# Kernel tuning notes

Hardware: AMD Instinct MI355X
Metric: run time of the kernel (lower is better)

Reference implementation:

```python
import jax, jax.numpy as jnp
import numpy as np

NUM_HEADS = 16
SOFTPLUS_EPS = 1e-4


def rotate_half(x):
    x1, x2 = jnp.split(x, 2, axis=-1)
    return jnp.concatenate((-x2, x1), axis=-1)


def setup_inputs() -> dict:
    key = jax.random.key(0)
    B, S, H = 1, 2048, 2048
    D = H // NUM_HEADS  # 128
    ks = jax.random.split(key, 5)
    hidden_states = jax.random.normal(ks[0], (B, S, H), dtype=jnp.float32)
    # standard RoPE tables: [S, D]
    inv_freq = 1.0 / (10000.0 ** (np.arange(0, D, 2, dtype=np.float32) / D))
    freqs = np.outer(np.arange(S, dtype=np.float32), inv_freq)  # [S, D/2]
    emb = np.concatenate([freqs, freqs], axis=-1)  # [S, D]
    cos = jnp.asarray(np.cos(emb), dtype=jnp.float32)
    sin = jnp.asarray(np.sin(emb), dtype=jnp.float32)
    std = 0.02
    w_q = jax.random.normal(ks[1], (2 * H, H), dtype=jnp.float32) * std
    w_k = jax.random.normal(ks[2], (2 * H, H), dtype=jnp.float32) * std
    w_v = jax.random.normal(ks[3], (H, H), dtype=jnp.float32) * std
    w_o = jax.random.normal(ks[4], (H, H), dtype=jnp.float32) * std
    return {"hidden_states": hidden_states, "cos": cos, "sin": sin,
            "w_q": w_q, "w_k": w_k, "w_v": w_v, "w_o": w_o}


def reference(hidden_states, cos, sin, w_q, w_k, w_v, w_o):
    B, S, H = hidden_states.shape
    NH = NUM_HEADS
    D = H // NH
    # projections (torch Linear: y = x @ W.T)
    q = (hidden_states @ w_q.T).reshape(B, S, NH, 2 * D).swapaxes(1, 2)  # [B,NH,S,2D]
    k = (hidden_states @ w_k.T).reshape(B, S, NH, 2 * D).swapaxes(1, 2)
    v = (hidden_states @ w_v.T).reshape(B, S, NH, D).swapaxes(1, 2)      # [B,NH,S,D]
    q_mu, q_sigma_raw = jnp.split(q, 2, axis=-1)
    k_mu, k_sigma_raw = jnp.split(k, 2, axis=-1)
    q_sigma = jax.nn.softplus(q_sigma_raw) + SOFTPLUS_EPS
    k_sigma = jax.nn.softplus(k_sigma_raw) + SOFTPLUS_EPS
    q_w = q_mu / jnp.sqrt(q_sigma)
    k_w = k_mu / jnp.sqrt(k_sigma)
    # RoPE on variance-weighted means; cos/sin [S,D] broadcast over [B,NH,S,D]
    q_w = q_w * cos + rotate_half(q_w) * sin
    k_w = k_w * cos + rotate_half(k_w) * sin
    q_sq = jnp.sum(q_w * q_w, axis=-1, keepdims=True)          # [B,NH,S,1]
    k_sq = jnp.sum(k_w * k_w, axis=-1, keepdims=True)          # [B,NH,S,1]
    dot = jnp.einsum('bhqd,bhkd->bhqk', q_w, k_w)              # [B,NH,S,S]
    weighted_dist = q_sq + jnp.swapaxes(k_sq, -2, -1) - 2.0 * dot
    log_det_q = jnp.sum(jnp.log(q_sigma), axis=-1, keepdims=True)
    log_det_k = jnp.sum(jnp.log(k_sigma), axis=-1, keepdims=True)
    log_det = log_det_q + jnp.swapaxes(log_det_k, -2, -1)
    attn_scores = -0.5 * (weighted_dist + log_det)
    attn_probs = jax.nn.softmax(attn_scores, axis=-1)
    attn_out = jnp.einsum('bhqk,bhkd->bhqd', attn_probs, v)    # [B,NH,S,D]
    attn_out = attn_out.swapaxes(1, 2).reshape(B, S, H)
    return attn_out @ w_o.T
```

## Files before the change

kernel.cpp:

```cpp
#include <hip/hip_runtime.h>
#include <stdint.h>

#define S_LEN 2048
#define HID   2048
#define NHEAD 16
#define HD    128
#define NQK   8192
#define K_HID 2048

typedef _Float16 f16x8 __attribute__((ext_vector_type(8)));
typedef float    f32x4 __attribute__((ext_vector_type(4)));

__device__ __forceinline__ unsigned short f2h(float f) {
    _Float16 h = (_Float16)f;
    union { _Float16 h; unsigned short u; } c; c.h = h;
    return c.u;
}
__device__ __forceinline__ float h2f(unsigned short b) {
    union { unsigned short u; _Float16 h; } c; c.u = b;
    return (float)c.h;
}
__device__ __forceinline__ float softplus_f(float x) {
    return (x > 20.f) ? x : log1pf(expf(x));
}
__device__ __forceinline__ void gload_lds16(const unsigned short* g, unsigned short* l) {
    __builtin_amdgcn_global_load_lds(
        (const __attribute__((address_space(1))) unsigned int*)g,
        (__attribute__((address_space(3))) unsigned int*)l, 16, 0, 0);
}

__global__ __launch_bounds__(256) void cast5(const float* __restrict__ hs,
                                             const float* __restrict__ wq,
                                             const float* __restrict__ wk,
                                             const float* __restrict__ wv,
                                             const float* __restrict__ wo,
                                             unsigned short* __restrict__ hs16,
                                             unsigned short* __restrict__ wqk16,
                                             unsigned short* __restrict__ wv16,
                                             unsigned short* __restrict__ wo16) {
    int b = blockIdx.x;
    const float* src;
    unsigned short* dst;
    int i;
    if (b < 4096)       { src = hs; dst = hs16;                          i = b; }
    else if (b < 12288) { src = wq; dst = wqk16;                         i = b - 4096; }
    else if (b < 20480) { src = wk; dst = wqk16 + (size_t)4096 * K_HID;  i = b - 12288; }
    else if (b < 24576) { src = wv; dst = wv16;                          i = b - 20480; }
    else                { src = wo; dst = wo16;                          i = b - 24576; }
    int idx = i * 256 + threadIdx.x;
    float4 v = ((const float4*)src)[idx];
    ushort4 o;
    o.x = f2h(v.x); o.y = f2h(v.y); o.z = f2h(v.z); o.w = f2h(v.w);
    ((ushort4*)dst)[idx] = o;
}

template <bool OUT_F16>
__device__ __forceinline__ void gemm_body(const unsigned short* __restrict__ A,
                                          const unsigned short* __restrict__ B,
                                          void* __restrict__ Cv,
                                          int m0, int n0, int N,
                                          unsigned short* As, unsigned short* Bs) {
    const int t    = threadIdx.x;
    const int wave = t >> 6;
    const int lane = t & 63;
    const int wm   = wave >> 1, wn = wave & 1;
    const int lrow = lane & 15, quad = lane >> 4;
    const int srow = lane >> 2;
    const int scol = (lane & 3) * 8;

    f32x4 acc[4][4];
    for (int i = 0; i < 4; ++i)
        for (int j = 0; j < 4; ++j)
            acc[i][j] = (f32x4){0.f, 0.f, 0.f, 0.f};

    for (int k0 = 0; k0 < K_HID; k0 += 32) {
        for (int c = 0; c < 2; ++c) {
            int ch = wave * 2 + c;
            int row = ch * 16 + srow;
            gload_lds16(A + (size_t)(m0 + row) * K_HID + k0 + scol, &As[ch * 512]);
            gload_lds16(B + (size_t)(n0 + row) * K_HID + k0 + scol, &Bs[ch * 512]);
        }
        __syncthreads();

        f16x8 af[4], bfr[4];
        for (int tm = 0; tm < 4; ++tm)
            af[tm]  = *(const f16x8*)(&As[(wm * 64 + tm * 16 + lrow) * 32 + quad * 8]);
        for (int tn = 0; tn < 4; ++tn)
            bfr[tn] = *(const f16x8*)(&Bs[(wn * 64 + tn * 16 + lrow) * 32 + quad * 8]);
        for (int tm = 0; tm < 4; ++tm)
            for (int tn = 0; tn < 4; ++tn)
                acc[tm][tn] = __builtin_amdgcn_mfma_f32_16x16x32_f16(af[tm], bfr[tn], acc[tm][tn], 0, 0, 0);
        __syncthreads();
    }

    for (int tm = 0; tm < 4; ++tm)
        for (int tn = 0; tn < 4; ++tn) {
            int col = n0 + wn * 64 + tn * 16 + lrow;
            for (int r = 0; r < 4; ++r) {
                int row = m0 + wm * 64 + tm * 16 + quad * 4 + r;
                if (OUT_F16)
                    ((unsigned short*)Cv)[(size_t)row * N + col] = f2h(acc[tm][tn][r]);
                else
                    ((float*)Cv)[(size_t)row * N + col] = acc[tm][tn][r];
            }
        }
}

__global__ __launch_bounds__(256) void gemm_qkv(const unsigned short* __restrict__ hs16,
                                                const unsigned short* __restrict__ wqk16,
                                                const unsigned short* __restrict__ wv16,
                                                unsigned short* __restrict__ qk16,
                                                unsigned short* __restrict__ Vt) {
    __shared__ __align__(16) unsigned short As[128 * 32];
    __shared__ __align__(16) unsigned short Bs[128 * 32];
    int b = blockIdx.x;
    if (b < 1024) {
        gemm_body<true>(hs16, wqk16, qk16, (b >> 6) * 128, (b & 63) * 128, NQK, As, Bs);
    } else {
        b -= 1024;
        gemm_body<true>(wv16, hs16, Vt, (b >> 4) * 128, (b & 15) * 128, S_LEN, As, Bs);
    }
}

template <bool OUT_F16>
__global__ __launch_bounds__(256) void gemm_nt_f16(const unsigned short* __restrict__ A,
                                                   const unsigned short* __restrict__ B,
                                                   void* __restrict__ Cv,
                                                   int M, int N, int Kd) {
    __shared__ __align__(16) unsigned short As[128 * 32];
    __shared__ __align__(16) unsigned short Bs[128 * 32];
    gemm_body<OUT_F16>(A, B, Cv, blockIdx.y * 128, blockIdx.x * 128, N, As, Bs);
}

__global__ __launch_bounds__(256) void prep_qk(const unsigned short* __restrict__ qk,
                                               const float* __restrict__ cosb,
                                               const float* __restrict__ sinb,
                                               unsigned short* __restrict__ Q16,
                                               unsigned short* __restrict__ K16,
                                               float* __restrict__ kbias) {
    int gid  = blockIdx.x * 4 + (threadIdx.x >> 6);
    int lane = threadIdx.x & 63;
    int h = gid >> 11;
    int s = gid & 2047;
    int d1 = lane, d2 = lane + 64;
    const unsigned short* row = qk + (size_t)s * NQK;
    float c1 = cosb[s * HD + d1], c2 = cosb[s * HD + d2];
    float s1 = sinb[s * HD + d1], s2 = sinb[s * HD + d2];
    size_t ob = ((size_t)h * S_LEN + s) * HD;

    {
        int base = h * 256;
        float mu1 = h2f(row[base + d1]),       mu2 = h2f(row[base + d2]);
        float sg1 = softplus_f(h2f(row[base + 128 + d1])) + 1e-4f;
        float sg2 = softplus_f(h2f(row[base + 128 + d2])) + 1e-4f;
        float w1 = mu1 * rsqrtf(sg1), w2 = mu2 * rsqrtf(sg2);
        float o1 = w1 * c1 - w2 * s1;
        float o2 = w2 * c2 + w1 * s2;
        Q16[ob + d1] = f2h(o1);
        Q16[ob + d2] = f2h(o2);
    }
    {
        int base = 4096 + h * 256;
        float mu1 = h2f(row[base + d1]),       mu2 = h2f(row[base + d2]);
        float sg1 = softplus_f(h2f(row[base + 128 + d1])) + 1e-4f;
        float sg2 = softplus_f(h2f(row[base + 128 + d2])) + 1e-4f;
        float w1 = mu1 * rsqrtf(sg1), w2 = mu2 * rsqrtf(sg2);
        float o1 = w1 * c1 - w2 * s1;
        float o2 = w2 * c2 + w1 * s2;
        unsigned short k1 = f2h(o1), k2 = f2h(o2);
        K16[ob + d1] = k1; K16[ob + d2] = k2;
        float r1 = h2f(k1), r2 = h2f(k2);
        float part = r1 * r1 + r2 * r2 + logf(sg1) + logf(sg2);
        for (int off = 32; off > 0; off >>= 1) part += __shfl_down(part, off);
        if (lane == 0) kbias[(size_t)h * S_LEN + s] = -0.5f * part;
    }
}

__global__ __launch_bounds__(256, 2) void flash_mfma(const unsigned short* __restrict__ Q16,
                                                     const unsigned short* __restrict__ K16,
                                                     const unsigned short* __restrict__ Vt,
                                                     const float* __restrict__ kbias,
                                                     unsigned short* __restrict__ OP,
                                                     float* __restrict__ ML) {
    constexpr int LV = 72;
    __shared__ __align__(16) unsigned short Khs[4 * 64 * 32];
    __shared__ __align__(16) unsigned short Vts[2 * 128 * 32];
    __shared__ __align__(16) unsigned short Ps[128 * LV];
    __shared__ float kb[64];

    const int t    = threadIdx.x;
    const int h    = blockIdx.y;
    const int q0   = blockIdx.x * 128;
    const int kz   = blockIdx.z;
    const int wave = t >> 6;
    const int lane = t & 63;
    const int lrow = lane & 15, quad = lane >> 4;
    const int srow = lane >> 2;
    const int scol = (lane & 3) * 8;

    f16x8 qf[2][4];
    for (int m = 0; m < 2; ++m) {
        size_t rb = ((size_t)h * S_LEN + q0 + wave * 32 + m * 16 + lrow) * HD;
        for (int kk = 0; kk < 4; ++kk)
            qf[m][kk] = *(const f16x8*)(Q16 + rb + kk * 32 + quad * 8);
    }

    float mrow[2][4], lsum[2][4];
    f32x4 Ofr[2][8];
    for (int m = 0; m < 2; ++m)
        for (int r = 0; r < 4; ++r) { mrow[m][r] = -INFINITY; lsum[m][r] = 0.f; }
    for (int m = 0; m < 2; ++m)
        for (int d = 0; d < 8; ++d) Ofr[m][d] = (f32x4){0.f, 0.f, 0.f, 0.f};

    const int kbeg = kz * 1024;
    for (int k0 = kbeg; k0 < kbeg + 1024; k0 += 64) {
        {
            const unsigned short* kgb = K16 + ((size_t)h * S_LEN + k0) * HD;
            const unsigned short* vgb = Vt + ((size_t)h * HD) * S_LEN + k0;
            for (int c = 0; c < 4; ++c) {
                int ch = wave * 4 + c;
                int kk = ch >> 2;
                int r  = (ch & 3) * 16 + srow;
                gload_lds16(kgb + (size_t)r * HD + kk * 32 + scol, &Khs[ch * 512]);
                int kc = ch >> 3;
                int r2 = (ch & 7) * 16 + srow;
                gload_lds16(vgb + (size_t)r2 * S_LEN + kc * 32 + scol, &Vts[ch * 512]);
            }
            if (t < 64) kb[t] = kbias[(size_t)h * S_LEN + k0 + t];
        }
        __syncthreads();

        f32x4 sc[2][4];
        for (int m = 0; m < 2; ++m)
            for (int nt = 0; nt < 4; ++nt) sc[m][nt] = (f32x4){0.f, 0.f, 0.f, 0.f};
        for (int kk = 0; kk < 4; ++kk)
            for (int nt = 0; nt < 4; ++nt) {
                f16x8 khf = *(const f16x8*)(&Khs[kk * 2048 + (nt * 16 + lrow) * 32 + quad * 8]);
                sc[0][nt] = __builtin_amdgcn_mfma_f32_16x16x32_f16(qf[0][kk], khf, sc[0][nt], 0, 0, 0);
                sc[1][nt] = __builtin_amdgcn_mfma_f32_16x16x32_f16(qf[1][kk], khf, sc[1][nt], 0, 0, 0);
            }
        float kbn[4] = {kb[lrow], kb[16 + lrow], kb[32 + lrow], kb[48 + lrow]};

        for (int m = 0; m < 2; ++m)
            for (int r = 0; r < 4; ++r) {
                float s0 = sc[m][0][r] + kbn[0];
                float s1 = sc[m][1][r] + kbn[1];
                float s2 = sc[m][2][r] + kbn[2];
                float s3 = sc[m][3][r] + kbn[3];
                float mx = fmaxf(fmaxf(s0, s1), fmaxf(s2, s3));
                mx = fmaxf(mx, __shfl_xor(mx, 1));
                mx = fmaxf(mx, __shfl_xor(mx, 2));
                mx = fmaxf(mx, __shfl_xor(mx, 4));
                mx = fmaxf(mx, __shfl_xor(mx, 8));
                float mnew  = fmaxf(mrow[m][r], mx);
                float alpha = __expf(mrow[m][r] - mnew);
                mrow[m][r] = mnew;
                float p0 = __expf(s0 - mnew);
                float p1 = __expf(s1 - mnew);
                float p2 = __expf(s2 - mnew);
                float p3 = __expf(s3 - mnew);
                lsum[m][r] = lsum[m][r] * alpha + ((p0 + p1) + (p2 + p3));
                for (int d = 0; d < 8; ++d) Ofr[m][d][r] *= alpha;
                int prow = (wave * 32 + m * 16 + quad * 4 + r) * LV;
                Ps[prow + lrow]      = f2h(p0);
                Ps[prow + 16 + lrow] = f2h(p1);
                Ps[prow + 32 + lrow] = f2h(p2);
                Ps[prow + 48 + lrow] = f2h(p3);
            }

        for (int c = 0; c < 2; ++c) {
            f16x8 pa0 = *(const f16x8*)(&Ps[(wave * 32 + lrow) * LV + c * 32 + quad * 8]);
            f16x8 pa1 = *(const f16x8*)(&Ps[(wave * 32 + 16 + lrow) * LV + c * 32 + quad * 8]);
            for (int dt = 0; dt < 8; ++dt) {
                f16x8 vb = *(const f16x8*)(&Vts[c * 4096 + (dt * 16 + lrow) * 32 + quad * 8]);
                Ofr[0][dt] = __builtin_amdgcn_mfma_f32_16x16x32_f16(pa0, vb, Ofr[0][dt], 0, 0, 0);
                Ofr[1][dt] = __builtin_amdgcn_mfma_f32_16x16x32_f16(pa1, vb, Ofr[1][dt], 0, 0, 0);
            }
        }
        __syncthreads();
    }

    size_t obase = (size_t)(kz * NHEAD + h) * S_LEN;
    for (int m = 0; m < 2; ++m)
        for (int r = 0; r < 4; ++r) {
            float rs = lsum[m][r];
            rs += __shfl_xor(rs, 1);
            rs += __shfl_xor(rs, 2);
            rs += __shfl_xor(rs, 4);
            rs += __shfl_xor(rs, 8);
            int qrow = q0 + wave * 32 + m * 16 + quad * 4 + r;
            unsigned short* op = OP + (obase + qrow) * HD;
            for (int dt = 0; dt < 8; ++dt)
                op[dt * 16 + lrow] = f2h(Ofr[m][dt][r]);
            if (lrow == 0) {
                ML[(obase + qrow) * 2]     = mrow[m][r];
                ML[(obase + qrow) * 2 + 1] = rs;
            }
        }
}

__global__ __launch_bounds__(256) void flash_merge(const unsigned short* __restrict__ OP,
                                                   const float* __restrict__ ML,
                                                   unsigned short* __restrict__ Obf) {
    int row = blockIdx.x * 2 + (threadIdx.x >> 7);
    int d   = threadIdx.x & 127;
    int h = row >> 11, q = row & 2047;
    size_t i0 = (size_t)h * S_LEN + q;
    size_t i1 = (size_t)(NHEAD + h) * S_LEN + q;
    float m0 = ML[i0 * 2], l0 = ML[i0 * 2 + 1];
    float m1 = ML[i1 * 2], l1 = ML[i1 * 2 + 1];
    float mf = fmaxf(m0, m1);
    float w0 = __expf(m0 - mf), w1 = __expf(m1 - mf);
    float inv = 1.f / (l0 * w0 + l1 * w1);
    float o = (h2f(OP[i0 * HD + d]) * w0 + h2f(OP[i1 * HD + d]) * w1) * inv;
    Obf[(size_t)q * HID + h * HD + d] = f2h(o);
}

extern "C" void kernel_launch(void* const* d_in, const int* in_sizes, int n_in,
                              void* d_out, int out_size, void* d_ws, size_t ws_size,
                              hipStream_t stream) {
    const float* hs   = (const float*)d_in[0];
    const float* cosb = (const float*)d_in[1];
    const float* sinb = (const float*)d_in[2];
    const float* wq   = (const float*)d_in[3];
    const float* wk   = (const float*)d_in[4];
    const float* wv   = (const float*)d_in[5];
    const float* wo   = (const float*)d_in[6];
    float* out = (float*)d_out;
    char*  ws  = (char*)d_ws;

    unsigned short* w_qk16 = (unsigned short*)(ws);
    unsigned short* Q16    = (unsigned short*)(ws);
    unsigned short* K16    = (unsigned short*)(ws + 8388608);
    float*          kbias  = (float*)(ws + 16777216);
    unsigned short* qk16   = (unsigned short*)(ws + 33554432);
    unsigned short* OP     = (unsigned short*)(ws + 33554432);
    float*          ML     = (float*)(ws + 50331648);
    unsigned short* hs16   = (unsigned short*)(ws + 67108864);
    unsigned short* Obf    = (unsigned short*)(ws + 67108864);
    unsigned short* w_v16  = (unsigned short*)(ws + 75497472);
    unsigned short* w_o16  = (unsigned short*)(ws + 83886080);
    unsigned short* Vt     = (unsigned short*)(ws + 92274688);

    cast5<<<28672, 256, 0, stream>>>(hs, wq, wk, wv, wo, hs16, w_qk16, w_v16, w_o16);

    gemm_qkv<<<1280, 256, 0, stream>>>(hs16, w_qk16, w_v16, qk16, Vt);

    prep_qk<<<(NHEAD * S_LEN) / 4, 256, 0, stream>>>(qk16, cosb, sinb,
                                                     Q16, K16, kbias);
    flash_mfma<<<dim3(S_LEN / 128, NHEAD, 2), 256, 0, stream>>>(Q16, K16, Vt,
                                                                kbias, OP, ML);
    flash_merge<<<(NHEAD * S_LEN) / 2, 256, 0, stream>>>(OP, ML, Obf);
    gemm_nt_f16<false><<<dim3(16, 16), 256, 0, stream>>>(Obf, w_o16, out, S_LEN, HID, K_HID);
}
```

Baseline: 394.1 us.

## Add 256x256 double-buffered MFMA GEMM for QK projection with async LDS loads

Adds a new 512-thread kernel for the large QK projection GEMM that uses 256x256 output tiles, 128KB of dynamic LDS, and double-buffered global-to-LDS direct loads. Loads are interleaved with MFMA phases under s_setprio and a swizzled LDS layout, with grid remapping for L2 locality. The V projection now runs as a separate launch of the existing 128-tile GEMM. The goal is more data reuse per tile and overlap of memory with compute, at the cost of an extra launch, heavy register pressure (128 accumulator floats per thread), and lower occupancy.

Result: no change. 400.7 us (+1.7%).

```diff
diff --git a/kernel.cpp b/kernel.cpp
--- a/kernel.cpp
+++ b/kernel.cpp
@@ -28,6 +28,12 @@
         (const __attribute__((address_space(1))) unsigned int*)g,
         (__attribute__((address_space(3))) unsigned int*)l, 16, 0, 0);
 }
+__device__ __forceinline__ void bar() {
+    asm volatile("" ::: "memory");
+    __builtin_amdgcn_s_barrier();
+    asm volatile("" ::: "memory");
+}
+#define VMCNT(n) asm volatile("s_waitcnt vmcnt(" #n ")" ::: "memory")
 
 __global__ __launch_bounds__(256) void cast5(const float* __restrict__ hs,
                                              const float* __restrict__ wq,
@@ -130,6 +136,166 @@
     __shared__ __align__(16) unsigned short As[128 * 32];
     __shared__ __align__(16) unsigned short Bs[128 * 32];
     gemm_body<OUT_F16>(A, B, Cv, blockIdx.y * 128, blockIdx.x * 128, N, As, Bs);
+}
+
+__global__ __launch_bounds__(512, 2) void gemm256_qk(const unsigned short* __restrict__ A,
+                                                     const unsigned short* __restrict__ B,
+                                                     unsigned short* __restrict__ C) {
+    extern __shared__ __align__(16) unsigned short lds[];
+    const int t    = threadIdx.x;
+    const int wave = t >> 6;
+    const int lane = t & 63;
+    const int wm   = wave >> 2, wn = wave & 3;
+    const int lrow = lane & 15, quad = lane >> 4;
+
+    const int x  = blockIdx.x & 7;
+    const int sl = blockIdx.x >> 3;
+    const int tm = ((x >> 2) << 2) + (sl >> 3);
+    const int tn = ((x & 3) << 3) + (sl & 7);
+    const int m0 = tm << 8, n0 = tn << 8;
+
+    const int srow = lane >> 2;
+    const int scol = ((lane & 3) * 8) ^ ((lane >> 5) << 4);
+    const unsigned short* Ag = A + (size_t)(m0 + wave * 16 + srow) * K_HID + scol;
+    const unsigned short* Bg = B + (size_t)(n0 + wave * 16 + srow) * K_HID + scol;
+
+    const int swz = (lrow * 32 + quad * 8) ^ ((lrow >> 3) << 4);
+
+    f32x4 acc[8][4];
+    #pragma unroll
+    for (int i = 0; i < 8; ++i)
+        #pragma unroll
+        for (int j = 0; j < 4; ++j) acc[i][j] = (f32x4){0.f, 0.f, 0.f, 0.f};
+
+    {
+        unsigned short* la = lds + wave * 1024;
+        gload_lds16(Ag,               la);
+        gload_lds16(Ag + 32,          la + 512);
+        gload_lds16(Ag + 262144,      la + 8192);
+        gload_lds16(Ag + 262144 + 32, la + 8704);
+        unsigned short* lb = la + 16384;
+        gload_lds16(Bg,               lb);
+        gload_lds16(Bg + 32,          lb + 512);
+        gload_lds16(Bg + 262144,      lb + 8192);
+        gload_lds16(Bg + 262144 + 32, lb + 8704);
+    }
+
+    const int NT = K_HID / 64;
+    #pragma unroll 1
+    for (int t2 = 0; t2 < NT; ++t2) {
+        const int buf = t2 & 1;
+        const unsigned short* Lb = lds + buf * 32768;
+        unsigned short*       Ln = lds + (buf ^ 1) * 32768 + wave * 1024;
+        const int k1  = (t2 + 1) * 64;
+        const bool pre = (t2 < NT - 1);
+
+        f16x8 af[4][2], bf[2][2];
+
+        if (pre) {
+            gload_lds16(Ag + k1,               Ln);
+            gload_lds16(Ag + k1 + 32,          Ln + 512);
+            gload_lds16(Ag + 262144 + k1,      Ln + 8192);
+            gload_lds16(Ag + 262144 + k1 + 32, Ln + 8704);
+            VMCNT(4);
+        } else {
+            VMCNT(0);
+        }
+        bar();
+        #pragma unroll
+        for (int i = 0; i < 4; ++i) {
+            af[i][0] = *(const f16x8*)(Lb + (wm * 8 + i) * 1024 + swz);
+            af[i][1] = *(const f16x8*)(Lb + (wm * 8 + i) * 1024 + 512 + swz);
+        }
+        #pragma unroll
+        for (int j = 0; j < 2; ++j) {
+            bf[j][0] = *(const f16x8*)(Lb + 16384 + (wn * 4 + j) * 1024 + swz);
+            bf[j][1] = *(const f16x8*)(Lb + 16384 + (wn * 4 + j) * 1024 + 512 + swz);
+        }
+        __builtin_amdgcn_s_setprio(1);
+        #pragma unroll
+        for (int i = 0; i < 4; ++i)
+            #pragma unroll
+            for (int j = 0; j < 2; ++j) {
+                acc[i][j] = __builtin_amdgcn_mfma_f32_16x16x32_f16(af[i][0], bf[j][0], acc[i][j], 0, 0, 0);
+                acc[i][j] = __builtin_amdgcn_mfma_f32_16x16x32_f16(af[i][1], bf[j][1], acc[i][j], 0, 0, 0);
+            }
+        __builtin_amdgcn_s_setprio(0);
+        bar();
+
+        #pragma unroll
+        for (int j = 0; j < 2; ++j) {
+            bf[j][0] = *(const f16x8*)(Lb + 16384 + (wn * 4 + 2 + j) * 1024 + swz);
+            bf[j][1] = *(const f16x8*)(Lb + 16384 + (wn * 4 + 2 + j) * 1024 + 512 + swz);
+        }
+        if (pre) {
+            gload_lds16(Bg + k1,               Ln + 16384);
+            gload_lds16(Bg + k1 + 32,          Ln + 16896);
+            gload_lds16(Bg + 262144 + k1,      Ln + 24576);
+            gload_lds16(Bg + 262144 + k1 + 32, Ln + 25088);
+        }
+        bar();
+        __builtin_amdgcn_s_setprio(1);
+        #pragma unroll
+        for (int i = 0; i < 4; ++i)
+            #pragma unroll
+            for (int j = 0; j < 2; ++j) {
+                acc[i][2 + j] = __builtin_amdgcn_mfma_f32_16x16x32_f16(af[i][0], bf[j][0], acc[i][2 + j], 0, 0, 0);
+                acc[i][2 + j] = __builtin_amdgcn_mfma_f32_16x16x32_f16(af[i][1], bf[j][1], acc[i][2 + j], 0, 0, 0);
+            }
+        __builtin_amdgcn_s_setprio(0);
+        bar();
+
+        #pragma unroll
+        for (int i = 0; i < 4; ++i) {
+            af[i][0] = *(const f16x8*)(Lb + (wm * 8 + 4 + i) * 1024 + swz);
+            af[i][1] = *(const f16x8*)(Lb + (wm * 8 + 4 + i) * 1024 + 512 + swz);
+        }
+        #pragma unroll
+        for (int j = 0; j < 2; ++j) {
+            bf[j][0] = *(const f16x8*)(Lb + 16384 + (wn * 4 + j) * 1024 + swz);
+            bf[j][1] = *(const f16x8*)(Lb + 16384 + (wn * 4 + j) * 1024 + 512 + swz);
+        }
+        bar();
+        __builtin_amdgcn_s_setprio(1);
+        #pragma unroll
+        for (int i = 0; i < 4; ++i)
+            #pragma unroll
+            for (int j = 0; j < 2; ++j) {
+                acc[4 + i][j] = __builtin_amdgcn_mfma_f32_16x16x32_f16(af[i][0], bf[j][0], acc[4 + i][j], 0, 0, 0);
+                acc[4 + i][j] = __builtin_amdgcn_mfma_f32_16x16x32_f16(af[i][1], bf[j][1], acc[4 + i][j], 0, 0, 0);
+            }
+        __builtin_amdgcn_s_setprio(0);
+        bar();
+
+        #pragma unroll
+        for (int j = 0; j < 2; ++j) {
+            bf[j][0] = *(const f16x8*)(Lb + 16384 + (wn * 4 + 2 + j) * 1024 + swz);
+            bf[j][1] = *(const f16x8*)(Lb + 16384 + (wn * 4 + 2 + j) * 1024 + 512 + swz);
+        }
+        bar();
+        __builtin_amdgcn_s_setprio(1);
+        #pragma unroll
+        for (int i = 0; i < 4; ++i)
+            #pragma unroll
+            for (int j = 0; j < 2; ++j) {
+                acc[4 + i][2 + j] = __builtin_amdgcn_mfma_f32_16x16x32_f16(af[i][0], bf[j][0], acc[4 + i][2 + j], 0, 0, 0);
+                acc[4 + i][2 + j] = __builtin_amdgcn_mfma_f32_16x16x32_f16(af[i][1], bf[j][1], acc[4 + i][2 + j], 0, 0, 0);
+            }
+        __builtin_amdgcn_s_setprio(0);
+        bar();
+    }
+
+    #pragma unroll
+    for (int m = 0; m < 8; ++m)
+        #pragma unroll
+        for (int n = 0; n < 4; ++n) {
+            const int col = n0 + wn * 64 + n * 16 + lrow;
+            #pragma unroll
+            for (int r = 0; r < 4; ++r) {
+                const int row = m0 + wm * 128 + m * 16 + quad * 4 + r;
+                C[(size_t)row * NQK + col] = f2h(acc[m][n][r]);
+            }
+        }
 }
 
 __global__ __launch_bounds__(256) void prep_qk(const unsigned short* __restrict__ qk,
@@ -342,9 +508,22 @@
     unsigned short* w_o16  = (unsigned short*)(ws + 83886080);
     unsigned short* Vt     = (unsigned short*)(ws + 92274688);
 
+    static int use256 = -1;
+    if (use256 < 0) {
+        hipError_t e = hipFuncSetAttribute((const void*)gemm256_qk,
+                                           hipFuncAttributeMaxDynamicSharedMemorySize,
+                                           131072);
+        use256 = (e == hipSuccess) ? 1 : 0;
+    }
+
     cast5<<<28672, 256, 0, stream>>>(hs, wq, wk, wv, wo, hs16, w_qk16, w_v16, w_o16);
 
-    gemm_qkv<<<1280, 256, 0, stream>>>(hs16, w_qk16, w_v16, qk16, Vt);
+    if (use256) {
+        gemm256_qk<<<256, 512, 131072, stream>>>(hs16, w_qk16, qk16);
+        gemm_nt_f16<true><<<dim3(16, 16), 256, 0, stream>>>(w_v16, hs16, Vt, HID, S_LEN, K_HID);
+    } else {
+        gemm_qkv<<<1280, 256, 0, stream>>>(hs16, w_qk16, w_v16, qk16, Vt);
+    }
 
     prep_qk<<<(NHEAD * S_LEN) / 4, 256, 0, stream>>>(qk16, cosb, sinb,
                                                      Q16, K16, kbias);
```
